# Kernel tuning notes

Measured on AMD Instinct MI355X. Metric: run time of the kernel, lower is better.

## Reference

```python
import jax, jax.numpy as jnp
import numpy as np

N_NODES = 100_000
N_EDGES = 1_600_000
HIDDEN = 32


def setup_inputs() -> dict:
    key = jax.random.key(0)
    ks = jax.random.split(key, 8)
    pos = jax.random.normal(ks[0], (N_NODES, 3), dtype=jnp.float32)
    edge_index = jax.random.randint(ks[1], (2, N_EDGES), 0, N_NODES, dtype=jnp.int64)
    batch = jnp.zeros((N_NODES,), dtype=jnp.int64)
    # layer 1 MLP: Linear(3+3 -> 32) -> ReLU -> Linear(32 -> 32)
    W1 = jax.random.normal(ks[2], (6, HIDDEN), dtype=jnp.float32) * (1.0 / np.sqrt(6))
    b1 = jnp.zeros((HIDDEN,), dtype=jnp.float32)
    W2 = jax.random.normal(ks[3], (HIDDEN, HIDDEN), dtype=jnp.float32) * (1.0 / np.sqrt(HIDDEN))
    b2 = jnp.zeros((HIDDEN,), dtype=jnp.float32)
    # layer 2 MLP: Linear(32+3 -> 32) -> ReLU -> Linear(32 -> 32)
    W3 = jax.random.normal(ks[4], (HIDDEN + 3, HIDDEN), dtype=jnp.float32) * (1.0 / np.sqrt(HIDDEN + 3))
    b3 = jnp.zeros((HIDDEN,), dtype=jnp.float32)
    W4 = jax.random.normal(ks[5], (HIDDEN, HIDDEN), dtype=jnp.float32) * (1.0 / np.sqrt(HIDDEN))
    b4 = jnp.zeros((HIDDEN,), dtype=jnp.float32)
    return {"pos": pos, "edge_index": edge_index, "batch": batch,
            "W1": W1, "b1": b1, "W2": W2, "b2": b2,
            "W3": W3, "b3": b3, "W4": W4, "b4": b4}


def _pointnet_layer(h, rel, src, dst, n_nodes, Wa, ba, Wb, bb):
    # per-edge: concat(h_j, pos_j - pos_i) -> Linear -> ReLU -> Linear, then max-scatter into i
    e = jnp.concatenate([h[src], rel], axis=-1)             # [E, in+3]
    m = jax.nn.relu(e @ Wa + ba) @ Wb + bb                  # [E, out]
    agg = jax.ops.segment_max(m, dst, num_segments=n_nodes)  # [N, out], -inf for isolated nodes
    return jnp.where(jnp.isfinite(agg), agg, 0.0)


def reference(pos, edge_index, batch, W1, b1, W2, b2, W3, b3, W4, b4):
    src = edge_index[0]  # j (source)
    dst = edge_index[1]  # i (target, aggregation index)
    n_nodes = pos.shape[0]
    rel = pos[src] - pos[dst]  # [E, 3]
    h = jax.nn.relu(_pointnet_layer(pos, rel, src, dst, n_nodes, W1, b1, W2, b2))
    h = jax.nn.relu(_pointnet_layer(h, rel, src, dst, n_nodes, W3, b3, W4, b4))
    return h
```

## Files before the change

kernel.cpp:

```cpp
#include <hip/hip_runtime.h>
#include <hip/hip_bf16.h>
#include <stdint.h>


#define BS 256
#define K1_EDGES 4096
#define P2_CAP 3072

typedef float v2f __attribute__((ext_vector_type(2)));
typedef __attribute__((ext_vector_type(8))) short bf16x8;
typedef __attribute__((ext_vector_type(16))) float f32x16;
typedef __bf16 bf16v2 __attribute__((ext_vector_type(2)));

__device__ __forceinline__ unsigned ordenc(float f) {
    unsigned u = __float_as_uint(f);
    return (u & 0x80000000u) ? ~u : (u | 0x80000000u);
}
__device__ __forceinline__ float orddec(unsigned o) {
    unsigned u = (o & 0x80000000u) ? (o ^ 0x80000000u) : ~o;
    return __uint_as_float(u);
}
#define ORD_NEG_INF 0x007FFFFFu

__device__ __forceinline__ unsigned cvt2(float x, float y) {
    v2f v = {x, y};
    bf16v2 b = __builtin_convertvector(v, bf16v2);
    return __builtin_bit_cast(unsigned, b);
}
__device__ __forceinline__ float bflo(unsigned u) { return __uint_as_float(u << 16); }
__device__ __forceinline__ float bfhi(unsigned u) { return __uint_as_float(u & 0xFFFF0000u); }


__global__ __launch_bounds__(BS) void init_kernel(unsigned* __restrict__ a,
                                                  unsigned* __restrict__ b, int n32) {
    int i = blockIdx.x * BS + threadIdx.x;
    if (i < n32) {
        a[i] = ORD_NEG_INF;
        b[i] = ORD_NEG_INF;
    }
}

__global__ __launch_bounds__(BS) void finalize_kernel(unsigned* __restrict__ buf, int n) {
    int i = blockIdx.x * BS + threadIdx.x;
    if (i < n) {
        float v = orddec(buf[i]);
        reinterpret_cast<float*>(buf)[i] = fmaxf(v, 0.0f);
    }
}

__global__ __launch_bounds__(BS) void bucket_hist_kernel(const int* __restrict__ ei, int E,
                                                         int NRP, int* __restrict__ blockHist) {
    __shared__ int hist[1024];
    const int tid = threadIdx.x;
    for (int r = tid; r < 1024; r += BS) hist[r] = 0;
    __syncthreads();
    const int base = blockIdx.x * K1_EDGES;
    const int M = min(K1_EDGES, E - base);
    for (int i = tid; i < M; i += BS) atomicAdd(&hist[ei[E + base + i] >> 7], 1);
    __syncthreads();
    for (int r = tid; r < NRP; r += BS) blockHist[blockIdx.x * NRP + r] = hist[r];
}

__global__ __launch_bounds__(512) void off_scan_kernel(const int* __restrict__ blockHist,
                                                       int NB1, int NRP,
                                                       int* __restrict__ off,
                                                       int* __restrict__ total) {
    const int r = (blockIdx.x * 512 + threadIdx.x) >> 6;
    const int lane = threadIdx.x & 63;
    if (r >= NRP) return;
    int carry = 0;
    const int chunks = (NB1 + 63) / 64;
    for (int c = 0; c < chunks; ++c) {
        const int b = c * 64 + lane;
        const int v = (b < NB1) ? blockHist[b * NRP + r] : 0;
        int x = v;
#pragma unroll
        for (int d = 1; d < 64; d <<= 1) {
            int y = __shfl_up(x, d, 64);
            if (lane >= d) x += y;
        }
        if (b < NB1) off[b * NRP + r] = carry + (x - v);
        carry += __shfl(x, 63, 64);
    }
    if (lane == 0) total[r] = carry;
}

__global__ __launch_bounds__(1024) void range_scan_kernel(const int* __restrict__ total,
                                                          int NRP, int* __restrict__ rangeBase) {
    __shared__ int s[1024];
    const int t = threadIdx.x;
    const int v = (t < NRP) ? total[t] : 0;
    s[t] = v;
    __syncthreads();
    for (int off = 1; off < 1024; off <<= 1) {
        int add = (t >= off) ? s[t - off] : 0;
        __syncthreads();
        s[t] += add;
        __syncthreads();
    }
    if (t < NRP) rangeBase[t] = s[t] - v;
}

__global__ __launch_bounds__(BS) void bucket_scatter_kernel(
    const int* __restrict__ ei, int E, int NRP, const int* __restrict__ off,
    const int* __restrict__ rangeBase, int2* __restrict__ sedgeB) {
    __shared__ int2 stage[K1_EDGES];
    __shared__ unsigned short inv[K1_EDGES];
    __shared__ int hist[1024], start[1024], cursor[1024];
    __shared__ int ts[BS];
    const int tid = threadIdx.x;
    for (int r = tid; r < 1024; r += BS) hist[r] = 0;
    __syncthreads();
    const int base = blockIdx.x * K1_EDGES;
    const int M = min(K1_EDGES, E - base);
    for (int i = tid; i < M; i += BS) {
        const int2 p = make_int2(ei[base + i], ei[E + base + i]);
        stage[i] = p;
        atomicAdd(&hist[p.y >> 7], 1);
    }
    __syncthreads();
    {
        const int i0 = tid * 4;
        const int l0 = hist[i0], l1 = hist[i0 + 1], l2 = hist[i0 + 2], l3 = hist[i0 + 3];
        const int tsum = l0 + l1 + l2 + l3;
        ts[tid] = tsum;
        __syncthreads();
        for (int off2 = 1; off2 < BS; off2 <<= 1) {
            int add = (tid >= off2) ? ts[tid - off2] : 0;
            __syncthreads();
            ts[tid] += add;
            __syncthreads();
        }
        const int texcl = ts[tid] - tsum;
        start[i0] = texcl;
        start[i0 + 1] = texcl + l0;
        start[i0 + 2] = texcl + l0 + l1;
        start[i0 + 3] = texcl + l0 + l1 + l2;
        cursor[i0] = start[i0];
        cursor[i0 + 1] = start[i0 + 1];
        cursor[i0 + 2] = start[i0 + 2];
        cursor[i0 + 3] = start[i0 + 3];
    }
    __syncthreads();
    for (int i = tid; i < M; i += BS) {
        const int pos = atomicAdd(&cursor[stage[i].y >> 7], 1);
        inv[pos] = (unsigned short)i;
    }
    __syncthreads();
    const int* offb = off + blockIdx.x * NRP;
    for (int j = tid; j < M; j += BS) {
        const int2 p = stage[inv[j]];
        const int r = p.y >> 7;
        sedgeB[rangeBase[r] + offb[r] + (j - start[r])] = p;
    }
}

__global__ __launch_bounds__(BS) void bucket_sort_kernel(
    const int2* __restrict__ sedgeB, const int* __restrict__ rangeBase,
    const int* __restrict__ total, int N, int2* __restrict__ sedge, int* __restrict__ row_ptr,
    int* __restrict__ cnt) {
    __shared__ int2 stage[P2_CAP];
    __shared__ unsigned short inv[P2_CAP];
    __shared__ int hist[128], start[128], cursor[128];
    const int r = blockIdx.x;
    const int tid = threadIdx.x;
    const int base = rangeBase[r];
    const int M = total[r];
    const bool fast = (M <= P2_CAP);
    if (tid < 128) hist[tid] = 0;
    __syncthreads();
    if (fast) {
        for (int i = tid; i < M; i += BS) {
            const int2 p = sedgeB[base + i];
            stage[i] = p;
            atomicAdd(&hist[p.y & 127], 1);
        }
    } else {
        if (tid < 128) {
            int c = 0;
            for (int i = 0; i < M; ++i) c += ((sedgeB[base + i].y & 127) == tid);
            hist[tid] = c;
        }
    }
    __syncthreads();
    if (tid < 128) start[tid] = hist[tid];
    __syncthreads();
    for (int off2 = 1; off2 < 128; off2 <<= 1) {
        int add = 0;
        if (tid < 128 && tid >= off2) add = start[tid - off2];
        __syncthreads();
        if (tid < 128) start[tid] += add;
        __syncthreads();
    }
    if (tid < 128) {
        const int excl = start[tid] - hist[tid];
        start[tid] = excl;
        cursor[tid] = excl;
        const int node = r * 128 + tid;
        if (node < N) {
            row_ptr[node] = base + excl;
            cnt[node] = hist[tid];
        }
    }
    __syncthreads();
    if (fast) {
        for (int i = tid; i < M; i += BS) {
            const int pos = atomicAdd(&cursor[stage[i].y & 127], 1);
            inv[pos] = (unsigned short)i;
        }
        __syncthreads();
        for (int j = tid; j < M; j += BS) sedge[base + j] = stage[inv[j]];
    } else {
        if (tid < 128) {
            int c = base + start[tid];
            for (int i = 0; i < M; ++i) {
                const int2 p = sedgeB[base + i];
                if ((p.y & 127) == tid) sedge[c++] = p;
            }
        }
    }
}

__global__ __launch_bounds__(BS) void prep1_kernel(const float* __restrict__ pos,
                                                   const float* __restrict__ Wa,
                                                   const float* __restrict__ ba,
                                                   unsigned* __restrict__ Ubf,
                                                   float* __restrict__ V, int N) {
    int n = blockIdx.x * BS + threadIdx.x;
    if (n >= N) return;
    const float p[3] = {pos[3 * n], pos[3 * n + 1], pos[3 * n + 2]};
    v2f u[16], v[16];
#pragma unroll
    for (int g = 0; g < 16; ++g) {
        u[g] = *reinterpret_cast<const v2f*>(&ba[g * 2]);
        v2f z = {0.0f, 0.0f};
        v[g] = z;
    }
#pragma unroll
    for (int i = 0; i < 3; ++i) {
        const v2f f = {p[i], p[i]};
#pragma unroll
        for (int g = 0; g < 16; ++g) {
            const v2f wA = *reinterpret_cast<const v2f*>(&Wa[i * 32 + g * 2]);
            const v2f wB = *reinterpret_cast<const v2f*>(&Wa[(i + 3) * 32 + g * 2]);
            u[g] = __builtin_elementwise_fma(f, wA + wB, u[g]);
            v[g] = __builtin_elementwise_fma(f, wB, v[g]);
        }
    }
    uint4* Up = reinterpret_cast<uint4*>(Ubf + (size_t)n * 16);
    float4* Vp = reinterpret_cast<float4*>(V + (size_t)n * 32);
#pragma unroll
    for (int q = 0; q < 4; ++q) {
        uint4 o;
        o.x = cvt2(u[4 * q + 0].x, u[4 * q + 0].y);
        o.y = cvt2(u[4 * q + 1].x, u[4 * q + 1].y);
        o.z = cvt2(u[4 * q + 2].x, u[4 * q + 2].y);
        o.w = cvt2(u[4 * q + 3].x, u[4 * q + 3].y);
        Up[q] = o;
    }
#pragma unroll
    for (int q = 0; q < 8; ++q)
        Vp[q] = make_float4(v[2 * q].x, v[2 * q].y, v[2 * q + 1].x, v[2 * q + 1].y);
}

__global__ __launch_bounds__(BS) void prep2_kernel(const float* __restrict__ pos,
                                                   const unsigned* __restrict__ aggA,
                                                   const float* __restrict__ Wa,
                                                   const float* __restrict__ ba,
                                                   unsigned* __restrict__ Ubf,
                                                   float* __restrict__ V, int N) {
    int n = blockIdx.x * BS + threadIdx.x;
    if (n >= N) return;
    float h[32];
    const uint4* hp = reinterpret_cast<const uint4*>(aggA + (size_t)n * 32);
#pragma unroll
    for (int q = 0; q < 8; ++q) {
        uint4 t = hp[q];
        h[4 * q + 0] = fmaxf(orddec(t.x), 0.0f);
        h[4 * q + 1] = fmaxf(orddec(t.y), 0.0f);
        h[4 * q + 2] = fmaxf(orddec(t.z), 0.0f);
        h[4 * q + 3] = fmaxf(orddec(t.w), 0.0f);
    }
    const float p[3] = {pos[3 * n], pos[3 * n + 1], pos[3 * n + 2]};
    v2f u[16], v[16];
#pragma unroll
    for (int g = 0; g < 16; ++g) {
        u[g] = *reinterpret_cast<const v2f*>(&ba[g * 2]);
        v2f z = {0.0f, 0.0f};
        v[g] = z;
    }
#pragma unroll
    for (int i = 0; i < 32; ++i) {
        const v2f f = {h[i], h[i]};
#pragma unroll
        for (int g = 0; g < 16; ++g) {
            const v2f w = *reinterpret_cast<const v2f*>(&Wa[i * 32 + g * 2]);
            u[g] = __builtin_elementwise_fma(f, w, u[g]);
        }
    }
#pragma unroll
    for (int i = 0; i < 3; ++i) {
        const v2f f = {p[i], p[i]};
#pragma unroll
        for (int g = 0; g < 16; ++g) {
            const v2f w = *reinterpret_cast<const v2f*>(&Wa[(32 + i) * 32 + g * 2]);
            u[g] = __builtin_elementwise_fma(f, w, u[g]);
            v[g] = __builtin_elementwise_fma(f, w, v[g]);
        }
    }
    uint4* Up = reinterpret_cast<uint4*>(Ubf + (size_t)n * 16);
    float4* Vp = reinterpret_cast<float4*>(V + (size_t)n * 32);
#pragma unroll
    for (int q = 0; q < 4; ++q) {
        uint4 o;
        o.x = cvt2(u[4 * q + 0].x, u[4 * q + 0].y);
        o.y = cvt2(u[4 * q + 1].x, u[4 * q + 1].y);
        o.z = cvt2(u[4 * q + 2].x, u[4 * q + 2].y);
        o.w = cvt2(u[4 * q + 3].x, u[4 * q + 3].y);
        Up[q] = o;
    }
#pragma unroll
    for (int q = 0; q < 8; ++q)
        Vp[q] = make_float4(v[2 * q].x, v[2 * q].y, v[2 * q + 1].x, v[2 * q + 1].y);
}

__global__ __launch_bounds__(BS, 6) void edge_seg_kernel(
    const unsigned* __restrict__ Ubf, const float4* __restrict__ V,
    const int* __restrict__ row_ptr, const int* __restrict__ cnt,
    const int2* __restrict__ sedge, const float* __restrict__ Wb,
    const float* __restrict__ bb, unsigned* __restrict__ agg, int E) {
    __shared__ __align__(16) unsigned lds[5632];

    const int tid = threadIdx.x;
    const int k0 = blockIdx.x * BS;
    const int blockEnd = min(k0 + BS, E);
    const int k = min(k0 + tid, E - 1);

    {
        const int n = tid & 31;
        const int p = (tid >> 5) * 2;
        lds[5120 + n * 16 + p + 0] = cvt2(Wb[(2 * p + 0) * 32 + n], Wb[(2 * p + 1) * 32 + n]);
        lds[5120 + n * 16 + p + 1] = cvt2(Wb[(2 * p + 2) * 32 + n], Wb[(2 * p + 3) * 32 + n]);
    }

    const int2 ed = sedge[k];
    {
        const uint4* Up = reinterpret_cast<const uint4*>(Ubf + (size_t)ed.x * 16);
        const float4* Vp = V + (size_t)ed.y * 8;
        const uint4 U0 = Up[0];
        const uint4 U1 = Up[1];
        const uint4 U2 = Up[2];
        const uint4 U3 = Up[3];
        const unsigned uu[16] = {U0.x, U0.y, U0.z, U0.w, U1.x, U1.y, U1.z, U1.w,
                                 U2.x, U2.y, U2.z, U2.w, U3.x, U3.y, U3.z, U3.w};
#pragma unroll
        for (int q = 0; q < 8; ++q) {
            const float4 vb = Vp[q];
            const unsigned a = uu[2 * q + 0];
            const unsigned b = uu[2 * q + 1];
            const float h0 = fmaxf(bflo(a) - vb.x, 0.0f);
            const float h1 = fmaxf(bfhi(a) - vb.y, 0.0f);
            const float h2 = fmaxf(bflo(b) - vb.z, 0.0f);
            const float h3 = fmaxf(bfhi(b) - vb.w, 0.0f);
            lds[tid * 20 + 2 * q + 0] = cvt2(h0, h1);
            lds[tid * 20 + 2 * q + 1] = cvt2(h2, h3);
        }
    }
    __syncthreads();

    const int l = tid & 63;
    const int w = tid >> 6;
    const int half = l >> 5;
    const int ln = l & 31;
    const uint4* ldsv = reinterpret_cast<const uint4*>(lds);

    const int e0 = 64 * w + ln;
    const int e1 = e0 + 32;
    const uint4 au00 = ldsv[e0 * 5 + half];
    const uint4 au01 = ldsv[e0 * 5 + half + 2];
    const uint4 au10 = ldsv[e1 * 5 + half];
    const uint4 au11 = ldsv[e1 * 5 + half + 2];
    const uint4 bu0 = ldsv[1280 + ln * 4 + half];
    const uint4 bu1 = ldsv[1280 + ln * 4 + half + 2];
    const float bbn = bb[ln];
    __syncthreads();

    f32x16 c0, c1;
#pragma unroll
    for (int i = 0; i < 16; ++i) {
        c0[i] = bbn;
        c1[i] = bbn;
    }
    c0 = __builtin_amdgcn_mfma_f32_32x32x16_bf16(__builtin_bit_cast(bf16x8, au00),
                                                 __builtin_bit_cast(bf16x8, bu0), c0, 0, 0, 0);
    c0 = __builtin_amdgcn_mfma_f32_32x32x16_bf16(__builtin_bit_cast(bf16x8, au01),
                                                 __builtin_bit_cast(bf16x8, bu1), c0, 0, 0, 0);
    c1 = __builtin_amdgcn_mfma_f32_32x32x16_bf16(__builtin_bit_cast(bf16x8, au10),
                                                 __builtin_bit_cast(bf16x8, bu0), c1, 0, 0, 0);
    c1 = __builtin_amdgcn_mfma_f32_32x32x16_bf16(__builtin_bit_cast(bf16x8, au11),
                                                 __builtin_bit_cast(bf16x8, bu1), c1, 0, 0, 0);

#pragma unroll
    for (int k2 = 0; k2 < 8; ++k2) {
        const int rr = 2 * k2;
        const int er = 64 * w + (rr & 3) + 8 * (rr >> 2) + 4 * half;
        lds[ln * 130 + (er >> 1)] = cvt2(c0[rr], c0[rr + 1]);
        lds[ln * 130 + (er >> 1) + 16] = cvt2(c1[rr], c1[rr + 1]);
    }
    __syncthreads();

    const int d0 = sedge[k0].y;
    const int d1 = sedge[blockEnd - 1].y;
    const int nPairs = (d1 - d0 + 1) * 32;
    for (int idx = tid; idx < nPairs; idx += BS) {
        const int c = idx & 31;
        const int n = d0 + (idx >> 5);
        const int rs = row_ptr[n];
        const int re = rs + cnt[n];
        const int s0 = max(rs, k0) - k0;
        const int s1 = min(re, blockEnd) - k0;
        if (s0 >= s1) continue;
        const unsigned* smc = &lds[c * 130];
        v2f m0 = {-INFINITY, -INFINITY};
        v2f m1 = m0;
        int e = s0;
        if (e & 1) {
            const unsigned u = smc[e >> 1];
            m0.x = fmaxf(m0.x, bfhi(u));
            ++e;
        }
        for (; e + 4 <= s1; e += 4) {
            const unsigned ua = smc[e >> 1];
            const unsigned ub = smc[(e >> 1) + 1];
            const v2f a = {bflo(ua), bfhi(ua)};
            const v2f b = {bflo(ub), bfhi(ub)};
            m0 = __builtin_elementwise_max(m0, a);
            m1 = __builtin_elementwise_max(m1, b);
        }
        if (e + 2 <= s1) {
            const unsigned u = smc[e >> 1];
            const v2f a = {bflo(u), bfhi(u)};
            m0 = __builtin_elementwise_max(m0, a);
            e += 2;
        }
        if (e < s1) m0.x = fmaxf(m0.x, bflo(smc[e >> 1]));
        const v2f mm = __builtin_elementwise_max(m0, m1);
        const float v = fmaxf(mm.x, mm.y);
        unsigned* p = &agg[(size_t)n * 32 + c];
        const unsigned enc = ordenc(v);
        if (rs >= k0 && re <= blockEnd)
            *p = enc;
        else
            atomicMax(p, enc);
    }
}

extern "C" void kernel_launch(void* const* d_in, const int* in_sizes, int n_in,
                              void* d_out, int out_size, void* d_ws, size_t ws_size,
                              hipStream_t stream) {
    const float* pos = (const float*)d_in[0];
    const int* ei = (const int*)d_in[1];
    const float* W1 = (const float*)d_in[3];
    const float* b1 = (const float*)d_in[4];
    const float* W2 = (const float*)d_in[5];
    const float* b2 = (const float*)d_in[6];
    const float* W3 = (const float*)d_in[7];
    const float* b3 = (const float*)d_in[8];
    const float* W4 = (const float*)d_in[9];
    const float* b4 = (const float*)d_in[10];

    const int E = in_sizes[1] / 2;
    const int N = in_sizes[0] / 3;
    const int n32 = N * 32;
    const int NPAD = ((N + BS - 1) / BS) * BS;
    const int EB = (E + BS - 1) / BS;
    const int NR = (N + 127) / 128;
    const int NRP = ((NR + 15) / 16) * 16;
    const int NB1 = (E + K1_EDGES - 1) / K1_EDGES;
    const int BH = NB1 * NRP;

    int* cnt = (int*)d_ws;
    int* row_ptr = cnt + NPAD;
    int* blockHist = row_ptr + NPAD;
    int* off = blockHist + BH;
    int* total = off + BH;
    int* rangeBase = total + NRP;
    int2* sedge = (int2*)(rangeBase + NRP);
    unsigned* aggA = (unsigned*)(sedge + E);
    unsigned* Ubf = aggA + n32;
    float* Vbuf = (float*)(Ubf + (size_t)NPAD * 16);
    int2* sedgeB = (int2*)Ubf;
    unsigned* aggB = (unsigned*)d_out;

    const int gridN32 = (n32 + BS - 1) / BS;
    const int NBn = (N + BS - 1) / BS;

    init_kernel<<<gridN32, BS, 0, stream>>>(aggA, aggB, n32);

    bucket_hist_kernel<<<NB1, BS, 0, stream>>>(ei, E, NRP, blockHist);
    off_scan_kernel<<<(NRP * 64 + 511) / 512, 512, 0, stream>>>(blockHist, NB1, NRP, off,
                                                                total);
    range_scan_kernel<<<1, 1024, 0, stream>>>(total, NRP, rangeBase);
    bucket_scatter_kernel<<<NB1, BS, 0, stream>>>(ei, E, NRP, off, rangeBase, sedgeB);
    bucket_sort_kernel<<<NR, BS, 0, stream>>>(sedgeB, rangeBase, total, N, sedge, row_ptr, cnt);

    prep1_kernel<<<NBn, BS, 0, stream>>>(pos, W1, b1, Ubf, Vbuf, N);
    edge_seg_kernel<<<EB, BS, 0, stream>>>(Ubf, (const float4*)Vbuf, row_ptr, cnt, sedge, W2,
                                           b2, aggA, E);
    prep2_kernel<<<NBn, BS, 0, stream>>>(pos, aggA, W3, b3, Ubf, Vbuf, N);
    edge_seg_kernel<<<EB, BS, 0, stream>>>(Ubf, (const float4*)Vbuf, row_ptr, cnt, sedge, W4,
                                           b4, aggB, E);
    finalize_kernel<<<gridN32, BS, 0, stream>>>(aggB, n32);
}
```

Before: 232.6 us.

## Fuse histogram, prep1 and init into one launch; double edge block size

Result: no change. 230.7 us (-0.8%).

```diff
diff --git a/kernel.cpp b/kernel.cpp
--- a/kernel.cpp
+++ b/kernel.cpp
@@ -4,6 +4,7 @@
 
 
 #define BS 256
+#define EBS 512
 #define K1_EDGES 4096
 #define P2_CAP 3072
 
@@ -30,13 +31,64 @@
 __device__ __forceinline__ float bflo(unsigned u) { return __uint_as_float(u << 16); }
 __device__ __forceinline__ float bfhi(unsigned u) { return __uint_as_float(u & 0xFFFF0000u); }
 
-
-__global__ __launch_bounds__(BS) void init_kernel(unsigned* __restrict__ a,
-                                                  unsigned* __restrict__ b, int n32) {
-    int i = blockIdx.x * BS + threadIdx.x;
-    if (i < n32) {
-        a[i] = ORD_NEG_INF;
-        b[i] = ORD_NEG_INF;
+__global__ __launch_bounds__(BS) void setup_kernel(
+    const int* __restrict__ ei, int E, int NRP, int* __restrict__ blockHist,
+    const float* __restrict__ pos, const float* __restrict__ Wa, const float* __restrict__ ba,
+    unsigned* __restrict__ Ubf, float* __restrict__ V, int N, unsigned* __restrict__ aggA,
+    unsigned* __restrict__ aggB, int n32, int NB1, int NBn) {
+    __shared__ int hist[1024];
+    const int tid = threadIdx.x;
+    const int b = blockIdx.x;
+    if (b < NB1) {
+        for (int r = tid; r < 1024; r += BS) hist[r] = 0;
+        __syncthreads();
+        const int base = b * K1_EDGES;
+        const int M = min(K1_EDGES, E - base);
+        for (int i = tid; i < M; i += BS) atomicAdd(&hist[ei[E + base + i] >> 7], 1);
+        __syncthreads();
+        for (int r = tid; r < NRP; r += BS) blockHist[b * NRP + r] = hist[r];
+    } else if (b < NB1 + NBn) {
+        const int n = (b - NB1) * BS + tid;
+        if (n >= N) return;
+        const float p[3] = {pos[3 * n], pos[3 * n + 1], pos[3 * n + 2]};
+        v2f u[16], v[16];
+#pragma unroll
+        for (int g = 0; g < 16; ++g) {
+            u[g] = *reinterpret_cast<const v2f*>(&ba[g * 2]);
+            v2f z = {0.0f, 0.0f};
+            v[g] = z;
+        }
+#pragma unroll
+        for (int i = 0; i < 3; ++i) {
+            const v2f f = {p[i], p[i]};
+#pragma unroll
+            for (int g = 0; g < 16; ++g) {
+                const v2f wA = *reinterpret_cast<const v2f*>(&Wa[i * 32 + g * 2]);
+                const v2f wB = *reinterpret_cast<const v2f*>(&Wa[(i + 3) * 32 + g * 2]);
+                u[g] = __builtin_elementwise_fma(f, wA + wB, u[g]);
+                v[g] = __builtin_elementwise_fma(f, wB, v[g]);
+            }
+        }
+        uint4* Up = reinterpret_cast<uint4*>(Ubf + (size_t)n * 16);
+        float4* Vp = reinterpret_cast<float4*>(V + (size_t)n * 32);
+#pragma unroll
+        for (int q = 0; q < 4; ++q) {
+            uint4 o;
+            o.x = cvt2(u[4 * q + 0].x, u[4 * q + 0].y);
+            o.y = cvt2(u[4 * q + 1].x, u[4 * q + 1].y);
+            o.z = cvt2(u[4 * q + 2].x, u[4 * q + 2].y);
+            o.w = cvt2(u[4 * q + 3].x, u[4 * q + 3].y);
+            Up[q] = o;
+        }
+#pragma unroll
+        for (int q = 0; q < 8; ++q)
+            Vp[q] = make_float4(v[2 * q].x, v[2 * q].y, v[2 * q + 1].x, v[2 * q + 1].y);
+    } else {
+        const int i = (b - NB1 - NBn) * BS + tid;
+        if (i < n32) {
+            aggA[i] = ORD_NEG_INF;
+            aggB[i] = ORD_NEG_INF;
+        }
     }
 }
 
@@ -46,19 +98,6 @@
         float v = orddec(buf[i]);
         reinterpret_cast<float*>(buf)[i] = fmaxf(v, 0.0f);
     }
-}
-
-__global__ __launch_bounds__(BS) void bucket_hist_kernel(const int* __restrict__ ei, int E,
-                                                         int NRP, int* __restrict__ blockHist) {
-    __shared__ int hist[1024];
-    const int tid = threadIdx.x;
-    for (int r = tid; r < 1024; r += BS) hist[r] = 0;
-    __syncthreads();
-    const int base = blockIdx.x * K1_EDGES;
-    const int M = min(K1_EDGES, E - base);
-    for (int i = tid; i < M; i += BS) atomicAdd(&hist[ei[E + base + i] >> 7], 1);
-    __syncthreads();
-    for (int r = tid; r < NRP; r += BS) blockHist[blockIdx.x * NRP + r] = hist[r];
 }
 
 __global__ __launch_bounds__(512) void off_scan_kernel(const int* __restrict__ blockHist,
@@ -221,48 +260,6 @@
     }
 }
 
-__global__ __launch_bounds__(BS) void prep1_kernel(const float* __restrict__ pos,
-                                                   const float* __restrict__ Wa,
-                                                   const float* __restrict__ ba,
-                                                   unsigned* __restrict__ Ubf,
-                                                   float* __restrict__ V, int N) {
-    int n = blockIdx.x * BS + threadIdx.x;
-    if (n >= N) return;
-    const float p[3] = {pos[3 * n], pos[3 * n + 1], pos[3 * n + 2]};
-    v2f u[16], v[16];
-#pragma unroll
-    for (int g = 0; g < 16; ++g) {
-        u[g] = *reinterpret_cast<const v2f*>(&ba[g * 2]);
-        v2f z = {0.0f, 0.0f};
-        v[g] = z;
-    }
-#pragma unroll
-    for (int i = 0; i < 3; ++i) {
-        const v2f f = {p[i], p[i]};
-#pragma unroll
-        for (int g = 0; g < 16; ++g) {
-            const v2f wA = *reinterpret_cast<const v2f*>(&Wa[i * 32 + g * 2]);
-            const v2f wB = *reinterpret_cast<const v2f*>(&Wa[(i + 3) * 32 + g * 2]);
-            u[g] = __builtin_elementwise_fma(f, wA + wB, u[g]);
-            v[g] = __builtin_elementwise_fma(f, wB, v[g]);
-        }
-    }
-    uint4* Up = reinterpret_cast<uint4*>(Ubf + (size_t)n * 16);
-    float4* Vp = reinterpret_cast<float4*>(V + (size_t)n * 32);
-#pragma unroll
-    for (int q = 0; q < 4; ++q) {
-        uint4 o;
-        o.x = cvt2(u[4 * q + 0].x, u[4 * q + 0].y);
-        o.y = cvt2(u[4 * q + 1].x, u[4 * q + 1].y);
-        o.z = cvt2(u[4 * q + 2].x, u[4 * q + 2].y);
-        o.w = cvt2(u[4 * q + 3].x, u[4 * q + 3].y);
-        Up[q] = o;
-    }
-#pragma unroll
-    for (int q = 0; q < 8; ++q)
-        Vp[q] = make_float4(v[2 * q].x, v[2 * q].y, v[2 * q + 1].x, v[2 * q + 1].y);
-}
-
 __global__ __launch_bounds__(BS) void prep2_kernel(const float* __restrict__ pos,
                                                    const unsigned* __restrict__ aggA,
                                                    const float* __restrict__ Wa,
@@ -324,23 +321,23 @@
         Vp[q] = make_float4(v[2 * q].x, v[2 * q].y, v[2 * q + 1].x, v[2 * q + 1].y);
 }
 
-__global__ __launch_bounds__(BS, 6) void edge_seg_kernel(
+__global__ __launch_bounds__(EBS, 6) void edge_seg_kernel(
     const unsigned* __restrict__ Ubf, const float4* __restrict__ V,
     const int* __restrict__ row_ptr, const int* __restrict__ cnt,
     const int2* __restrict__ sedge, const float* __restrict__ Wb,
     const float* __restrict__ bb, unsigned* __restrict__ agg, int E) {
-    __shared__ __align__(16) unsigned lds[5632];
+    __shared__ __align__(16) unsigned lds[10752];
 
     const int tid = threadIdx.x;
-    const int k0 = blockIdx.x * BS;
-    const int blockEnd = min(k0 + BS, E);
+    const int k0 = blockIdx.x * EBS;
+    const int blockEnd = min(k0 + EBS, E);
     const int k = min(k0 + tid, E - 1);
 
-    {
+    if (tid < 256) {
         const int n = tid & 31;
         const int p = (tid >> 5) * 2;
-        lds[5120 + n * 16 + p + 0] = cvt2(Wb[(2 * p + 0) * 32 + n], Wb[(2 * p + 1) * 32 + n]);
-        lds[5120 + n * 16 + p + 1] = cvt2(Wb[(2 * p + 2) * 32 + n], Wb[(2 * p + 3) * 32 + n]);
+        lds[10240 + n * 16 + p + 0] = cvt2(Wb[(2 * p + 0) * 32 + n], Wb[(2 * p + 1) * 32 + n]);
+        lds[10240 + n * 16 + p + 1] = cvt2(Wb[(2 * p + 2) * 32 + n], Wb[(2 * p + 3) * 32 + n]);
     }
 
     const int2 ed = sedge[k];
@@ -380,8 +377,8 @@
     const uint4 au01 = ldsv[e0 * 5 + half + 2];
     const uint4 au10 = ldsv[e1 * 5 + half];
     const uint4 au11 = ldsv[e1 * 5 + half + 2];
-    const uint4 bu0 = ldsv[1280 + ln * 4 + half];
-    const uint4 bu1 = ldsv[1280 + ln * 4 + half + 2];
+    const uint4 bu0 = ldsv[2560 + ln * 4 + half];
+    const uint4 bu1 = ldsv[2560 + ln * 4 + half + 2];
     const float bbn = bb[ln];
     __syncthreads();
 
@@ -404,15 +401,15 @@
     for (int k2 = 0; k2 < 8; ++k2) {
         const int rr = 2 * k2;
         const int er = 64 * w + (rr & 3) + 8 * (rr >> 2) + 4 * half;
-        lds[ln * 130 + (er >> 1)] = cvt2(c0[rr], c0[rr + 1]);
-        lds[ln * 130 + (er >> 1) + 16] = cvt2(c1[rr], c1[rr + 1]);
+        lds[ln * 258 + (er >> 1)] = cvt2(c0[rr], c0[rr + 1]);
+        lds[ln * 258 + (er >> 1) + 16] = cvt2(c1[rr], c1[rr + 1]);
     }
     __syncthreads();
 
     const int d0 = sedge[k0].y;
     const int d1 = sedge[blockEnd - 1].y;
     const int nPairs = (d1 - d0 + 1) * 32;
-    for (int idx = tid; idx < nPairs; idx += BS) {
+    for (int idx = tid; idx < nPairs; idx += EBS) {
         const int c = idx & 31;
         const int n = d0 + (idx >> 5);
         const int rs = row_ptr[n];
@@ -420,7 +417,7 @@
         const int s0 = max(rs, k0) - k0;
         const int s1 = min(re, blockEnd) - k0;
         if (s0 >= s1) continue;
-        const unsigned* smc = &lds[c * 130];
+        const unsigned* smc = &lds[c * 258];
         v2f m0 = {-INFINITY, -INFINITY};
         v2f m1 = m0;
         int e = s0;
@@ -473,7 +470,7 @@
     const int N = in_sizes[0] / 3;
     const int n32 = N * 32;
     const int NPAD = ((N + BS - 1) / BS) * BS;
-    const int EB = (E + BS - 1) / BS;
+    const int EB2 = (E + EBS - 1) / EBS;
     const int NR = (N + 127) / 128;
     const int NRP = ((NR + 15) / 16) * 16;
     const int NB1 = (E + K1_EDGES - 1) / K1_EDGES;
@@ -486,29 +483,28 @@
     int* total = off + BH;
     int* rangeBase = total + NRP;
     int2* sedge = (int2*)(rangeBase + NRP);
-    unsigned* aggA = (unsigned*)(sedge + E);
+    int2* sedgeB = sedge + E;
+    unsigned* aggA = (unsigned*)(sedgeB + E);
     unsigned* Ubf = aggA + n32;
     float* Vbuf = (float*)(Ubf + (size_t)NPAD * 16);
-    int2* sedgeB = (int2*)Ubf;
     unsigned* aggB = (unsigned*)d_out;
 
     const int gridN32 = (n32 + BS - 1) / BS;
     const int NBn = (N + BS - 1) / BS;
 
-    init_kernel<<<gridN32, BS, 0, stream>>>(aggA, aggB, n32);
-
-    bucket_hist_kernel<<<NB1, BS, 0, stream>>>(ei, E, NRP, blockHist);
+    setup_kernel<<<NB1 + NBn + gridN32, BS, 0, stream>>>(ei, E, NRP, blockHist, pos, W1, b1,
+                                                         Ubf, Vbuf, N, aggA, aggB, n32, NB1,
+                                                         NBn);
     off_scan_kernel<<<(NRP * 64 + 511) / 512, 512, 0, stream>>>(blockHist, NB1, NRP, off,
                                                                 total);
     range_scan_kernel<<<1, 1024, 0, stream>>>(total, NRP, rangeBase);
     bucket_scatter_kernel<<<NB1, BS, 0, stream>>>(ei, E, NRP, off, rangeBase, sedgeB);
     bucket_sort_kernel<<<NR, BS, 0, stream>>>(sedgeB, rangeBase, total, N, sedge, row_ptr, cnt);
 
-    prep1_kernel<<<NBn, BS, 0, stream>>>(pos, W1, b1, Ubf, Vbuf, N);
-    edge_seg_kernel<<<EB, BS, 0, stream>>>(Ubf, (const float4*)Vbuf, row_ptr, cnt, sedge, W2,
-                                           b2, aggA, E);
+    edge_seg_kernel<<<EB2, EBS, 0, stream>>>(Ubf, (const float4*)Vbuf, row_ptr, cnt, sedge, W2,
+                                             b2, aggA, E);
     prep2_kernel<<<NBn, BS, 0, stream>>>(pos, aggA, W3, b3, Ubf, Vbuf, N);
-    edge_seg_kernel<<<EB, BS, 0, stream>>>(Ubf, (const float4*)Vbuf, row_ptr, cnt, sedge, W4,
-                                           b4, aggB, E);
+    edge_seg_kernel<<<EB2, EBS, 0, stream>>>(Ubf, (const float4*)Vbuf, row_ptr, cnt, sedge, W4,
+                                             b4, aggB, E);
     finalize_kernel<<<gridN32, BS, 0, stream>>>(aggB, n32);
 }
```
